# Kernel tuning notes

Hardware: AMD Instinct MI355X
Metric: run time of the kernel (lower is better)

The kernel has to match this reference:

```python
import jax, jax.numpy as jnp
import numpy as np

N_NODES = 50000
N_EDGES = 800000
D = 128        # in_channels == out_channels
EDGE_DIM = 32
EPS = 0.0      # GINEConv default eps


def setup_inputs() -> dict:
    key = jax.random.key(0)
    ks = jax.random.split(key, 12)
    s = lambda d: 1.0 / np.sqrt(d)
    inp = {
        "x": jax.random.normal(ks[0], (N_NODES, D), jnp.float32),
        "edge_index": jax.random.randint(ks[1], (2, N_EDGES), 0, N_NODES, jnp.int64),
        "edge_attr": jax.random.normal(ks[2], (N_EDGES, EDGE_DIM), jnp.float32),
        "importance": jax.random.uniform(ks[3], (N_NODES, 1), jnp.float32),
        # GINEConv edge lin: Linear(edge_dim, in_channels)
        "We": jax.random.uniform(ks[4], (EDGE_DIM, D), jnp.float32, -s(EDGE_DIM), s(EDGE_DIM)),
        "be": jax.random.uniform(ks[5], (D,), jnp.float32, -s(EDGE_DIM), s(EDGE_DIM)),
        # GINEConv nn: Linear(in_channels, out_channels)
        "Wc": jax.random.uniform(ks[6], (D, D), jnp.float32, -s(D), s(D)),
        "bc": jax.random.uniform(ks[7], (D,), jnp.float32, -s(D), s(D)),
        # importance_gate: Linear(out_channels + 1, out_channels)
        "Wg": jax.random.uniform(ks[8], (D + 1, D), jnp.float32, -s(D + 1), s(D + 1)),
        "bg": jax.random.uniform(ks[9], (D,), jnp.float32, -s(D + 1), s(D + 1)),
        # importance_propagation: Linear(out_channels, 1)
        "Wp": jax.random.uniform(ks[10], (D, 1), jnp.float32, -s(D), s(D)),
        "bp": jax.random.uniform(ks[11], (1,), jnp.float32, -s(D), s(D)),
    }
    return inp


def reference(x, edge_index, edge_attr, importance, We, be, Wc, bc, Wg, bg, Wp, bp):
    src, dst = edge_index[0], edge_index[1]
    # GINEConv: messages = relu(x_j + lin(edge_attr)), aggregated by sum at dst
    e = edge_attr @ We + be                      # [E, D]
    msg = jax.nn.relu(x[src] + e)                # [E, D] gather + fused add/relu
    agg = jax.ops.segment_sum(msg, dst, num_segments=N_NODES)  # [N, D] scatter-add
    conv_out = ((1.0 + EPS) * x + agg) @ Wc + bc  # [N, D]
    # importance gating + residual
    gate_in = jnp.concatenate([conv_out, importance], axis=-1)  # [N, D+1]
    gate = jax.nn.sigmoid(gate_in @ Wg + bg)
    out = gate * conv_out + (1.0 - gate) * x
    propagated_importance = out @ Wp + bp        # [N, 1]
    return (out, propagated_importance)
```

## Files before the change

### kernel.cpp

```cpp
#include <hip/hip_runtime.h>

#define NN 50000
#define NE 800000
#define DD 128
#define ED 32
#define NB 196
#define NC32 (NE / 32)

typedef short  bf16x8 __attribute__((ext_vector_type(8)));
typedef short  s16x8  __attribute__((ext_vector_type(8)));
typedef float  f32x4  __attribute__((ext_vector_type(4)));
typedef float  f32x16 __attribute__((ext_vector_type(16)));

__device__ __forceinline__ float4 ld4(const float* p) {
    return *reinterpret_cast<const float4*>(p);
}
__device__ __forceinline__ short f2bf(float f) {
    unsigned u = __float_as_uint(f);
    u += 0x7fffu + ((u >> 16) & 1u);
    return (short)(u >> 16);
}
__device__ __forceinline__ float bf2f(short h) {
    return __uint_as_float(((unsigned)(unsigned short)h) << 16);
}
__device__ __forceinline__ int sniff64(const int* ei) {
    return ((ei[1] | ei[3] | ei[5] | ei[7]) == 0) ? 1 : 0;
}

__global__ __launch_bounds__(256)
void k_xcast(const float* __restrict__ x, unsigned short* __restrict__ xb) {
    const int t = blockIdx.x * 256 + threadIdx.x;
    const int base = t * 8;
    const float4 a = ld4(x + base), b = ld4(x + base + 4);
    s16x8 o;
    o[0] = f2bf(a.x); o[1] = f2bf(a.y); o[2] = f2bf(a.z); o[3] = f2bf(a.w);
    o[4] = f2bf(b.x); o[5] = f2bf(b.y); o[6] = f2bf(b.z); o[7] = f2bf(b.w);
    *reinterpret_cast<s16x8*>(xb + base) = o;
}

__global__ __launch_bounds__(256)
void k_hist(const int* __restrict__ ei, int* __restrict__ counts) {
    const int is64 = sniff64(ei);
    for (int e = blockIdx.x * blockDim.x + threadIdx.x; e < NE;
         e += gridDim.x * blockDim.x) {
        const int dst = ei[(long)(NE + e) << is64];
        atomicAdd(&counts[dst], 1);
    }
}

__global__ __launch_bounds__(256)
void k_bsum(const int* __restrict__ counts, int* __restrict__ bsum) {
    const int i = blockIdx.x * 256 + threadIdx.x;
    int c = (i < NN) ? counts[i] : 0;
#pragma unroll
    for (int off = 32; off; off >>= 1) c += __shfl_xor(c, off, 64);
    __shared__ int ws4[4];
    if ((threadIdx.x & 63) == 0) ws4[threadIdx.x >> 6] = c;
    __syncthreads();
    if (threadIdx.x == 0) bsum[blockIdx.x] = ws4[0] + ws4[1] + ws4[2] + ws4[3];
}

__global__ __launch_bounds__(256)
void k_scanb(const int* __restrict__ bsum, int* __restrict__ bexcl) {
    const int tid = threadIdx.x, lane = tid & 63, w = tid >> 6;
    const int v = (tid < NB) ? bsum[tid] : 0;
    int s = v;
#pragma unroll
    for (int off = 1; off < 64; off <<= 1) {
        const int t = __shfl_up(s, off, 64);
        if (lane >= off) s += t;
    }
    __shared__ int wsum[4], wexcl[4];
    if (lane == 63) wsum[w] = s;
    __syncthreads();
    if (tid == 0) {
        int r = 0;
#pragma unroll
        for (int k = 0; k < 4; ++k) { wexcl[k] = r; r += wsum[k]; }
    }
    __syncthreads();
    if (tid < NB) bexcl[tid] = wexcl[w] + s - v;
}

__global__ __launch_bounds__(256)
void k_rowptr(const int* __restrict__ counts, const int* __restrict__ bexcl,
              int* __restrict__ cursor) {
    const int tid = threadIdx.x, lane = tid & 63, w = tid >> 6;
    const int i = blockIdx.x * 256 + tid;
    const int c = (i < NN) ? counts[i] : 0;
    int s = c;
#pragma unroll
    for (int off = 1; off < 64; off <<= 1) {
        const int t = __shfl_up(s, off, 64);
        if (lane >= off) s += t;
    }
    __shared__ int wsum[4], wexcl[4];
    if (lane == 63) wsum[w] = s;
    __syncthreads();
    if (tid == 0) {
        int r = 0;
#pragma unroll
        for (int k = 0; k < 4; ++k) { wexcl[k] = r; r += wsum[k]; }
    }
    __syncthreads();
    if (i < NN) cursor[i] = bexcl[blockIdx.x] + wexcl[w] + s - c;
}

__global__ __launch_bounds__(256)
void k_scatter(const int* __restrict__ ei, int* __restrict__ cursor,
               int2* __restrict__ sdat, int* __restrict__ edst) {
    const int is64 = sniff64(ei);
    for (int e = blockIdx.x * blockDim.x + threadIdx.x; e < NE;
         e += gridDim.x * blockDim.x) {
        const int src = ei[(long)e << is64];
        const int dst = ei[(long)(NE + e) << is64];
        const int pos = atomicAdd(&cursor[dst], 1);
        sdat[pos] = make_int2(src, e);
        edst[pos] = dst;
    }
}

__global__ __launch_bounds__(256, 4)
void k_aggE(const unsigned short* __restrict__ xb, const float* __restrict__ ea,
            const float* __restrict__ We, const float* __restrict__ be,
            const int2* __restrict__ sdat, const int* __restrict__ edst,
            float* __restrict__ agg)
{
    const int lane = threadIdx.x & 63;
    const int col  = lane & 31;
    const int h    = lane >> 5;
    const int wid  = (blockIdx.x << 2) | (threadIdx.x >> 6);
    if (wid >= NC32) return;

    bf16x8 Bf[4][2];
    float  beb[4];
#pragma unroll
    for (int bb = 0; bb < 4; ++bb) {
#pragma unroll
        for (int s = 0; s < 2; ++s)
#pragma unroll
            for (int i = 0; i < 8; ++i)
                Bf[bb][s][i] = f2bf(We[(s * 16 + h * 8 + i) * DD + bb * 32 + col]);
        beb[bb] = be[bb * 32 + col];
    }

    const int2 dv   = sdat[wid * 32 + col];
    const int  dstv = edst[wid * 32 + col];

    unsigned off[16];
#pragma unroll
    for (int reg = 0; reg < 16; ++reg) {
        const int E = (reg & 3) + 8 * (reg >> 2) + 4 * h;
        const int src = __shfl(dv.x, E, 64);
        off[reg] = (unsigned)src * DD + col;
    }

    f32x16 C[4];
#pragma unroll
    for (int bb = 0; bb < 4; ++bb)
#pragma unroll
        for (int reg = 0; reg < 16; ++reg)
            C[bb][reg] = __uint_as_float((unsigned)xb[off[reg] + bb * 32] << 16);

    const float* ear = ea + (size_t)dv.y * ED + h * 8;
    const float4 a00 = ld4(ear),      a01 = ld4(ear + 4);
    const float4 a10 = ld4(ear + 16), a11 = ld4(ear + 20);
    bf16x8 Af0, Af1;
    Af0[0] = f2bf(a00.x); Af0[1] = f2bf(a00.y); Af0[2] = f2bf(a00.z); Af0[3] = f2bf(a00.w);
    Af0[4] = f2bf(a01.x); Af0[5] = f2bf(a01.y); Af0[6] = f2bf(a01.z); Af0[7] = f2bf(a01.w);
    Af1[0] = f2bf(a10.x); Af1[1] = f2bf(a10.y); Af1[2] = f2bf(a10.z); Af1[3] = f2bf(a10.w);
    Af1[4] = f2bf(a11.x); Af1[5] = f2bf(a11.y); Af1[6] = f2bf(a11.z); Af1[7] = f2bf(a11.w);

#pragma unroll
    for (int bb = 0; bb < 4; ++bb) {
        C[bb] = __builtin_amdgcn_mfma_f32_32x32x16_bf16(Af0, Bf[bb][0], C[bb], 0, 0, 0);
        C[bb] = __builtin_amdgcn_mfma_f32_32x32x16_bf16(Af1, Bf[bb][1], C[bb], 0, 0, 0);
    }

#pragma unroll
    for (int bb = 0; bb < 4; ++bb)
#pragma unroll
        for (int reg = 0; reg < 16; ++reg)
            C[bb][reg] = fmaxf(C[bb][reg] + beb[bb], 0.0f);

    const int  prv  = __shfl(dstv, (col == 0) ? 0 : col - 1, 64);
    const bool flag = (lane < 32) && ((col == 0) || (dstv != prv));
    unsigned rem = (unsigned)(__ballot(flag) & 0xFFFFFFFFull);

    while (rem) {
        const int ms = __ffs((int)rem) - 1;
        rem &= rem - 1;
        const int hi = rem ? (__ffs((int)rem) - 1) : 32;
        const int d  = __shfl(dstv, ms, 64);

        float v0 = 0.f, v1 = 0.f, v2 = 0.f, v3 = 0.f;
#pragma unroll
        for (int reg = 0; reg < 16; ++reg) {
            const int E = (reg & 3) + 8 * (reg >> 2) + 4 * h;
            const float mk = (E >= ms && E < hi) ? 1.0f : 0.0f;
            v0 = fmaf(mk, C[0][reg], v0);
            v1 = fmaf(mk, C[1][reg], v1);
            v2 = fmaf(mk, C[2][reg], v2);
            v3 = fmaf(mk, C[3][reg], v3);
        }
        v0 += __shfl_xor(v0, 32, 64);
        v1 += __shfl_xor(v1, 32, 64);
        v2 += __shfl_xor(v2, 32, 64);
        v3 += __shfl_xor(v3, 32, 64);

        float* ar = agg + (size_t)d * DD + h * 64 + col;
        unsafeAtomicAdd(ar,      h ? v2 : v0);
        unsafeAtomicAdd(ar + 32, h ? v3 : v1);
    }
}

__global__ __launch_bounds__(256)
void k_conv(const float* __restrict__ x, const float* agg,
            const float* __restrict__ Wc, const float* __restrict__ bc,
            float* conv)
{
    __shared__ short sBh[2048 * 8];
    __shared__ short sBl[2048 * 8];
    for (int idx = threadIdx.x; idx < 2048; idx += 256) {
        const int kk = idx >> 9;
        const int b  = (idx >> 6) & 7;
        const int l  = idx & 63;
        const int row0 = kk * 32 + ((l >> 4) << 3);
        const int col  = b * 16 + (l & 15);
        bf16x8 h8, l8;
#pragma unroll
        for (int j = 0; j < 8; ++j) {
            const float v = Wc[(row0 + j) * DD + col];
            const short h = f2bf(v);
            h8[j] = h;
            l8[j] = f2bf(v - bf2f(h));
        }
        *reinterpret_cast<bf16x8*>(&sBh[idx * 8]) = h8;
        *reinterpret_cast<bf16x8*>(&sBl[idx * 8]) = l8;
    }
    __syncthreads();

    const int lane = threadIdx.x & 63;
    const int ncol = lane & 15;
    const int krow = (lane >> 4) << 3;
    const int grp  = lane >> 4;
    const int wid  = (blockIdx.x << 2) | (threadIdx.x >> 6);
    if (wid >= NN / 16) return;

    float bcb[8];
#pragma unroll
    for (int b = 0; b < 8; ++b) bcb[b] = bc[b * 16 + ncol];

    const int m0 = wid * 16;
    const float* xrow = x   + (size_t)(m0 + ncol) * DD + krow;
    const float* grow = agg + (size_t)(m0 + ncol) * DD + krow;

    f32x4 C[8];
#pragma unroll
    for (int b = 0; b < 8; ++b) {
        f32x4 c = { bcb[b], bcb[b], bcb[b], bcb[b] };
        C[b] = c;
    }

#pragma unroll
    for (int kk = 0; kk < 4; ++kk) {
        const float4 x0 = ld4(xrow + kk * 32), x1 = ld4(xrow + kk * 32 + 4);
        const float4 g0 = ld4(grow + kk * 32), g1 = ld4(grow + kk * 32 + 4);
        const float av[8] = { x0.x + g0.x, x0.y + g0.y, x0.z + g0.z, x0.w + g0.w,
                              x1.x + g1.x, x1.y + g1.y, x1.z + g1.z, x1.w + g1.w };
        bf16x8 Ah, Al;
#pragma unroll
        for (int j = 0; j < 8; ++j) {
            const short h = f2bf(av[j]);
            Ah[j] = h;
            Al[j] = f2bf(av[j] - bf2f(h));
        }
#pragma unroll
        for (int b = 0; b < 8; ++b) {
            const bf16x8 Bh = *reinterpret_cast<const bf16x8*>(&sBh[((kk * 8 + b) * 64 + lane) * 8]);
            const bf16x8 Bl = *reinterpret_cast<const bf16x8*>(&sBl[((kk * 8 + b) * 64 + lane) * 8]);
            C[b] = __builtin_amdgcn_mfma_f32_16x16x32_bf16(Ah, Bh, C[b], 0, 0, 0);
            C[b] = __builtin_amdgcn_mfma_f32_16x16x32_bf16(Al, Bh, C[b], 0, 0, 0);
            C[b] = __builtin_amdgcn_mfma_f32_16x16x32_bf16(Ah, Bl, C[b], 0, 0, 0);
        }
    }

#pragma unroll
    for (int r = 0; r < 4; ++r) {
        float* crow = conv + (size_t)(m0 + (grp << 2) + r) * DD + ncol;
#pragma unroll
        for (int b = 0; b < 8; ++b) crow[b * 16] = C[b][r];
    }
}

__global__ __launch_bounds__(256)
void k_gate(const float* __restrict__ x, const float* conv,
            const float* __restrict__ imp, const float* __restrict__ Wg,
            const float* __restrict__ bg, const float* __restrict__ Wp,
            const float* __restrict__ bp, float* outp, float* __restrict__ prop)
{
    __shared__ short sBh[2048 * 8];
    __shared__ short sBl[2048 * 8];
    for (int idx = threadIdx.x; idx < 2048; idx += 256) {
        const int kk = idx >> 9;
        const int b  = (idx >> 6) & 7;
        const int l  = idx & 63;
        const int row0 = kk * 32 + ((l >> 4) << 3);
        const int col  = b * 16 + (l & 15);
        bf16x8 h8, l8;
#pragma unroll
        for (int j = 0; j < 8; ++j) {
            const float v = Wg[(row0 + j) * DD + col];
            const short h = f2bf(v);
            h8[j] = h;
            l8[j] = f2bf(v - bf2f(h));
        }
        *reinterpret_cast<bf16x8*>(&sBh[idx * 8]) = h8;
        *reinterpret_cast<bf16x8*>(&sBl[idx * 8]) = l8;
    }
    __syncthreads();

    const int lane = threadIdx.x & 63;
    const int ncol = lane & 15;
    const int krow = (lane >> 4) << 3;
    const int grp  = lane >> 4;
    const int wid  = (blockIdx.x << 2) | (threadIdx.x >> 6);
    if (wid >= NN / 16) return;

    float bgb[8], wgi[8], wp8[8];
#pragma unroll
    for (int b = 0; b < 8; ++b) {
        bgb[b] = bg[b * 16 + ncol];
        wgi[b] = Wg[DD * DD + b * 16 + ncol];
        wp8[b] = Wp[b * 16 + ncol];
    }
    const float bps = bp[0];

    const int m0 = wid * 16;

    float cvD[8][4], xvD[8][4], im[4];
#pragma unroll
    for (int r = 0; r < 4; ++r) {
        const int m = m0 + (grp << 2) + r;
        const float* cr = conv + (size_t)m * DD + ncol;
        const float* xr = x    + (size_t)m * DD + ncol;
        im[r] = imp[m];
#pragma unroll
        for (int b = 0; b < 8; ++b) { cvD[b][r] = cr[b * 16]; xvD[b][r] = xr[b * 16]; }
    }

    f32x4 C[8];
#pragma unroll
    for (int b = 0; b < 8; ++b) {
        f32x4 c = { bgb[b], bgb[b], bgb[b], bgb[b] };
        C[b] = c;
    }

    const float* arow = conv + (size_t)(m0 + ncol) * DD + krow;
#pragma unroll
    for (int kk = 0; kk < 4; ++kk) {
        const float4 a0 = ld4(arow + kk * 32);
        const float4 a1 = ld4(arow + kk * 32 + 4);
        const float av[8] = { a0.x, a0.y, a0.z, a0.w, a1.x, a1.y, a1.z, a1.w };
        bf16x8 Ah, Al;
#pragma unroll
        for (int j = 0; j < 8; ++j) {
            const short h = f2bf(av[j]);
            Ah[j] = h;
            Al[j] = f2bf(av[j] - bf2f(h));
        }
#pragma unroll
        for (int b = 0; b < 8; ++b) {
            const bf16x8 Bh = *reinterpret_cast<const bf16x8*>(&sBh[((kk * 8 + b) * 64 + lane) * 8]);
            const bf16x8 Bl = *reinterpret_cast<const bf16x8*>(&sBl[((kk * 8 + b) * 64 + lane) * 8]);
            C[b] = __builtin_amdgcn_mfma_f32_16x16x32_bf16(Ah, Bh, C[b], 0, 0, 0);
            C[b] = __builtin_amdgcn_mfma_f32_16x16x32_bf16(Al, Bh, C[b], 0, 0, 0);
            C[b] = __builtin_amdgcn_mfma_f32_16x16x32_bf16(Ah, Bl, C[b], 0, 0, 0);
        }
    }

    float s[4] = { 0.f, 0.f, 0.f, 0.f };
#pragma unroll
    for (int r = 0; r < 4; ++r) {
        float* orow = outp + (size_t)(m0 + (grp << 2) + r) * DD + ncol;
#pragma unroll
        for (int b = 0; b < 8; ++b) {
            const float a = C[b][r] + im[r] * wgi[b];
            const float g = 1.0f / (1.0f + expf(-a));
            const float o = fmaf(g, cvD[b][r] - xvD[b][r], xvD[b][r]);
            orow[b * 16] = o;
            s[r] += o * wp8[b];
        }
    }
#pragma unroll
    for (int off = 1; off < 16; off <<= 1) {
        s[0] += __shfl_xor(s[0], off, 64);
        s[1] += __shfl_xor(s[1], off, 64);
        s[2] += __shfl_xor(s[2], off, 64);
        s[3] += __shfl_xor(s[3], off, 64);
    }
    if (ncol < 4) {
        const float v = (ncol == 0) ? s[0] : (ncol == 1) ? s[1] : (ncol == 2) ? s[2] : s[3];
        prop[m0 + (grp << 2) + ncol] = v + bps;
    }
}

extern "C" void kernel_launch(void* const* d_in, const int* in_sizes, int n_in,
                              void* d_out, int out_size, void* d_ws, size_t ws_size,
                              hipStream_t stream) {
    const float* x   = (const float*)d_in[0];
    const int*   ei  = (const int*)d_in[1];
    const float* ea  = (const float*)d_in[2];
    const float* imp = (const float*)d_in[3];
    const float* We  = (const float*)d_in[4];
    const float* be  = (const float*)d_in[5];
    const float* Wc  = (const float*)d_in[6];
    const float* bc  = (const float*)d_in[7];
    const float* Wg  = (const float*)d_in[8];
    const float* bg  = (const float*)d_in[9];
    const float* Wp  = (const float*)d_in[10];
    const float* bp  = (const float*)d_in[11];

    float* out  = (float*)d_out;
    float* prop = out + (size_t)NN * DD;
    float* agg  = out;

    int*            counts = (int*)d_ws;
    int*            cursor = (int*)((char*)d_ws + 204800);
    int*            bsum   = (int*)((char*)d_ws + 409600);
    int*            bexcl  = (int*)((char*)d_ws + 413696);
    int2*           sdat   = (int2*)((char*)d_ws + 1048576);
    int*            edst   = (int*)((char*)d_ws + 7448576);
    unsigned short* xb     = (unsigned short*)((char*)d_ws + 10649600);

    hipMemsetAsync(counts, 0, NN * sizeof(int), stream);
    hipMemsetAsync(agg, 0, (size_t)NN * DD * sizeof(float), stream);
    hipLaunchKernelGGL(k_xcast,   dim3(3125), dim3(256), 0, stream, x, xb);
    hipLaunchKernelGGL(k_hist,    dim3(2048), dim3(256), 0, stream, ei, counts);
    hipLaunchKernelGGL(k_bsum,    dim3(NB),   dim3(256), 0, stream, counts, bsum);
    hipLaunchKernelGGL(k_scanb,   dim3(1),    dim3(256), 0, stream, bsum, bexcl);
    hipLaunchKernelGGL(k_rowptr,  dim3(NB),   dim3(256), 0, stream, counts, bexcl, cursor);
    hipLaunchKernelGGL(k_scatter, dim3(2048), dim3(256), 0, stream, ei, cursor, sdat, edst);
    hipLaunchKernelGGL(k_aggE,    dim3(6250), dim3(256), 0, stream,
                       xb, ea, We, be, sdat, edst, agg);
    hipLaunchKernelGGL(k_conv,    dim3(782),  dim3(256), 0, stream, x, agg, Wc, bc, out);
    hipLaunchKernelGGL(k_gate,    dim3(782),  dim3(256), 0, stream,
                       x, out, imp, Wg, bg, Wp, bp, out, prop);
}
```

Measured before the change: 221.2 us.

## Fuse conv and gate kernels, pack dst into sdat, interleave bf16 x layout

Merges the conv and gate GEMM kernels into one, keeping conv output in shared memory instead of a global round trip, and drops the lo-part split for the gate GEMM (bf16-only Wg). Packs the destination index into the upper 16 bits of the source field to remove the separate edst array. Rearranges bf16 x so each lane fetches its four column chunks with a single 8-byte load, and has each aggregation wave process two 32-edge chunks. The packing assumes node ids fit in 16 bits, but N is 50000, so dst<<16 can overflow the sign bit and the mask logic may misbehave, and gate precision drops.

```diff
diff --git a/kernel.cpp b/kernel.cpp
--- a/kernel.cpp
+++ b/kernel.cpp
@@ -6,6 +6,7 @@
 #define ED 32
 #define NB 196
 #define NC32 (NE / 32)
+#define NWAG 12500
 
 typedef short  bf16x8 __attribute__((ext_vector_type(8)));
 typedef short  s16x8  __attribute__((ext_vector_type(8)));
@@ -28,22 +29,26 @@
 }
 
 __global__ __launch_bounds__(256)
-void k_xcast(const float* __restrict__ x, unsigned short* __restrict__ xb) {
+void k_xcast(const float* __restrict__ x, unsigned int* __restrict__ xb) {
     const int t = blockIdx.x * 256 + threadIdx.x;
-    const int base = t * 8;
-    const float4 a = ld4(x + base), b = ld4(x + base + 4);
-    s16x8 o;
-    o[0] = f2bf(a.x); o[1] = f2bf(a.y); o[2] = f2bf(a.z); o[3] = f2bf(a.w);
-    o[4] = f2bf(b.x); o[5] = f2bf(b.y); o[6] = f2bf(b.z); o[7] = f2bf(b.w);
-    *reinterpret_cast<s16x8*>(xb + base) = o;
+    if (t >= NN * 32) return;
+    const int n = t >> 5, c = t & 31;
+    const float* xr = x + (size_t)n * DD + c;
+    const unsigned b0 = (unsigned short)f2bf(xr[0]);
+    const unsigned b1 = (unsigned short)f2bf(xr[32]);
+    const unsigned b2 = (unsigned short)f2bf(xr[64]);
+    const unsigned b3 = (unsigned short)f2bf(xr[96]);
+    xb[(size_t)n * 64 + c * 2]     = b0 | (b1 << 16);
+    xb[(size_t)n * 64 + c * 2 + 1] = b2 | (b3 << 16);
 }
 
 __global__ __launch_bounds__(256)
 void k_hist(const int* __restrict__ ei, int* __restrict__ counts) {
     const int is64 = sniff64(ei);
+    const int2* ei2 = (const int2*)ei;
     for (int e = blockIdx.x * blockDim.x + threadIdx.x; e < NE;
          e += gridDim.x * blockDim.x) {
-        const int dst = ei[(long)(NE + e) << is64];
+        const int dst = is64 ? ei2[NE + e].x : ei[NE + e];
         atomicAdd(&counts[dst], 1);
     }
 }
@@ -108,29 +113,28 @@
 
 __global__ __launch_bounds__(256)
 void k_scatter(const int* __restrict__ ei, int* __restrict__ cursor,
-               int2* __restrict__ sdat, int* __restrict__ edst) {
+               int2* __restrict__ sdat) {
     const int is64 = sniff64(ei);
+    const int2* ei2 = (const int2*)ei;
     for (int e = blockIdx.x * blockDim.x + threadIdx.x; e < NE;
          e += gridDim.x * blockDim.x) {
-        const int src = ei[(long)e << is64];
-        const int dst = ei[(long)(NE + e) << is64];
+        const int src = is64 ? ei2[e].x : ei[e];
+        const int dst = is64 ? ei2[NE + e].x : ei[NE + e];
         const int pos = atomicAdd(&cursor[dst], 1);
-        sdat[pos] = make_int2(src, e);
-        edst[pos] = dst;
+        sdat[pos] = make_int2(src | (dst << 16), e);
     }
 }
 
 __global__ __launch_bounds__(256, 4)
-void k_aggE(const unsigned short* __restrict__ xb, const float* __restrict__ ea,
+void k_aggE(const unsigned int* __restrict__ xb, const float* __restrict__ ea,
             const float* __restrict__ We, const float* __restrict__ be,
-            const int2* __restrict__ sdat, const int* __restrict__ edst,
-            float* __restrict__ agg)
+            const int2* __restrict__ sdat, float* __restrict__ agg)
 {
     const int lane = threadIdx.x & 63;
     const int col  = lane & 31;
     const int h    = lane >> 5;
     const int wid  = (blockIdx.x << 2) | (threadIdx.x >> 6);
-    if (wid >= NC32) return;
+    if (wid >= NWAG) return;
 
     bf16x8 Bf[4][2];
     float  beb[4];
@@ -144,80 +148,87 @@
         beb[bb] = be[bb * 32 + col];
     }
 
-    const int2 dv   = sdat[wid * 32 + col];
-    const int  dstv = edst[wid * 32 + col];
-
-    unsigned off[16];
-#pragma unroll
-    for (int reg = 0; reg < 16; ++reg) {
-        const int E = (reg & 3) + 8 * (reg >> 2) + 4 * h;
-        const int src = __shfl(dv.x, E, 64);
-        off[reg] = (unsigned)src * DD + col;
-    }
-
-    f32x16 C[4];
-#pragma unroll
-    for (int bb = 0; bb < 4; ++bb)
-#pragma unroll
-        for (int reg = 0; reg < 16; ++reg)
-            C[bb][reg] = __uint_as_float((unsigned)xb[off[reg] + bb * 32] << 16);
-
-    const float* ear = ea + (size_t)dv.y * ED + h * 8;
-    const float4 a00 = ld4(ear),      a01 = ld4(ear + 4);
-    const float4 a10 = ld4(ear + 16), a11 = ld4(ear + 20);
-    bf16x8 Af0, Af1;
-    Af0[0] = f2bf(a00.x); Af0[1] = f2bf(a00.y); Af0[2] = f2bf(a00.z); Af0[3] = f2bf(a00.w);
-    Af0[4] = f2bf(a01.x); Af0[5] = f2bf(a01.y); Af0[6] = f2bf(a01.z); Af0[7] = f2bf(a01.w);
-    Af1[0] = f2bf(a10.x); Af1[1] = f2bf(a10.y); Af1[2] = f2bf(a10.z); Af1[3] = f2bf(a10.w);
-    Af1[4] = f2bf(a11.x); Af1[5] = f2bf(a11.y); Af1[6] = f2bf(a11.z); Af1[7] = f2bf(a11.w);
-
-#pragma unroll
-    for (int bb = 0; bb < 4; ++bb) {
-        C[bb] = __builtin_amdgcn_mfma_f32_32x32x16_bf16(Af0, Bf[bb][0], C[bb], 0, 0, 0);
-        C[bb] = __builtin_amdgcn_mfma_f32_32x32x16_bf16(Af1, Bf[bb][1], C[bb], 0, 0, 0);
-    }
-
-#pragma unroll
-    for (int bb = 0; bb < 4; ++bb)
-#pragma unroll
-        for (int reg = 0; reg < 16; ++reg)
-            C[bb][reg] = fmaxf(C[bb][reg] + beb[bb], 0.0f);
-
-    const int  prv  = __shfl(dstv, (col == 0) ? 0 : col - 1, 64);
-    const bool flag = (lane < 32) && ((col == 0) || (dstv != prv));
-    unsigned rem = (unsigned)(__ballot(flag) & 0xFFFFFFFFull);
-
-    while (rem) {
-        const int ms = __ffs((int)rem) - 1;
-        rem &= rem - 1;
-        const int hi = rem ? (__ffs((int)rem) - 1) : 32;
-        const int d  = __shfl(dstv, ms, 64);
-
-        float v0 = 0.f, v1 = 0.f, v2 = 0.f, v3 = 0.f;
+    int2 dvs0 = sdat[(size_t)wid * 32 + col];
+    int2 dvs1 = sdat[(size_t)(wid + NWAG) * 32 + col];
+
+#pragma unroll
+    for (int k2 = 0; k2 < 2; ++k2) {
+        const int2 dv = k2 ? dvs1 : dvs0;
+
+        const float* ear = ea + (size_t)dv.y * ED + h * 8;
+        const float4 a00 = ld4(ear),      a01 = ld4(ear + 4);
+        const float4 a10 = ld4(ear + 16), a11 = ld4(ear + 20);
+
+        f32x16 C[4];
 #pragma unroll
         for (int reg = 0; reg < 16; ++reg) {
-            const int E = (reg & 3) + 8 * (reg >> 2) + 4 * h;
-            const float mk = (E >= ms && E < hi) ? 1.0f : 0.0f;
-            v0 = fmaf(mk, C[0][reg], v0);
-            v1 = fmaf(mk, C[1][reg], v1);
-            v2 = fmaf(mk, C[2][reg], v2);
-            v3 = fmaf(mk, C[3][reg], v3);
-        }
-        v0 += __shfl_xor(v0, 32, 64);
-        v1 += __shfl_xor(v1, 32, 64);
-        v2 += __shfl_xor(v2, 32, 64);
-        v3 += __shfl_xor(v3, 32, 64);
-
-        float* ar = agg + (size_t)d * DD + h * 64 + col;
-        unsafeAtomicAdd(ar,      h ? v2 : v0);
-        unsafeAtomicAdd(ar + 32, h ? v3 : v1);
-    }
-}
-
-__global__ __launch_bounds__(256)
-void k_conv(const float* __restrict__ x, const float* agg,
-            const float* __restrict__ Wc, const float* __restrict__ bc,
-            float* conv)
+            const int E   = (reg & 3) + 8 * (reg >> 2) + 4 * h;
+            const int src = __shfl(dv.x, E, 64) & 0xFFFF;
+            const uint2 w = *reinterpret_cast<const uint2*>(
+                                xb + (size_t)src * 64 + col * 2);
+            C[0][reg] = __uint_as_float(w.x << 16);
+            C[1][reg] = __uint_as_float(w.x & 0xFFFF0000u);
+            C[2][reg] = __uint_as_float(w.y << 16);
+            C[3][reg] = __uint_as_float(w.y & 0xFFFF0000u);
+        }
+
+        bf16x8 Af0, Af1;
+        Af0[0] = f2bf(a00.x); Af0[1] = f2bf(a00.y); Af0[2] = f2bf(a00.z); Af0[3] = f2bf(a00.w);
+        Af0[4] = f2bf(a01.x); Af0[5] = f2bf(a01.y); Af0[6] = f2bf(a01.z); Af0[7] = f2bf(a01.w);
+        Af1[0] = f2bf(a10.x); Af1[1] = f2bf(a10.y); Af1[2] = f2bf(a10.z); Af1[3] = f2bf(a10.w);
+        Af1[4] = f2bf(a11.x); Af1[5] = f2bf(a11.y); Af1[6] = f2bf(a11.z); Af1[7] = f2bf(a11.w);
+
+#pragma unroll
+        for (int bb = 0; bb < 4; ++bb) {
+            C[bb] = __builtin_amdgcn_mfma_f32_32x32x16_bf16(Af0, Bf[bb][0], C[bb], 0, 0, 0);
+            C[bb] = __builtin_amdgcn_mfma_f32_32x32x16_bf16(Af1, Bf[bb][1], C[bb], 0, 0, 0);
+        }
+
+#pragma unroll
+        for (int bb = 0; bb < 4; ++bb)
+#pragma unroll
+            for (int reg = 0; reg < 16; ++reg)
+                C[bb][reg] = fmaxf(C[bb][reg] + beb[bb], 0.0f);
+
+        const int  dstv = ((unsigned)dv.x) >> 16;
+        const int  prv  = __shfl(dstv, (lane == 0) ? 0 : lane - 1, 64);
+        const bool flag = (lane < 32) && ((col == 0) || (dstv != prv));
+        unsigned rem = (unsigned)(__ballot(flag) & 0xFFFFFFFFull);
+
+        while (rem) {
+            const int ms = __ffs((int)rem) - 1;
+            rem &= rem - 1;
+            const int hi = rem ? (__ffs((int)rem) - 1) : 32;
+            const int d  = __shfl(dstv, ms, 64);
+
+            float v0 = 0.f, v1 = 0.f, v2 = 0.f, v3 = 0.f;
+#pragma unroll
+            for (int reg = 0; reg < 16; ++reg) {
+                const int E = (reg & 3) + 8 * (reg >> 2) + 4 * h;
+                const float mk = (E >= ms && E < hi) ? 1.0f : 0.0f;
+                v0 = fmaf(mk, C[0][reg], v0);
+                v1 = fmaf(mk, C[1][reg], v1);
+                v2 = fmaf(mk, C[2][reg], v2);
+                v3 = fmaf(mk, C[3][reg], v3);
+            }
+            v0 += __shfl_xor(v0, 32, 64);
+            v1 += __shfl_xor(v1, 32, 64);
+            v2 += __shfl_xor(v2, 32, 64);
+            v3 += __shfl_xor(v3, 32, 64);
+
+            float* ar = agg + (size_t)d * DD + h * 64 + col;
+            unsafeAtomicAdd(ar,      h ? v2 : v0);
+            unsafeAtomicAdd(ar + 32, h ? v3 : v1);
+        }
+    }
+}
+
+__global__ __launch_bounds__(256)
+void k_cg(const float* __restrict__ x, const float* agg,
+          const float* __restrict__ Wc, const float* __restrict__ bc,
+          const float* __restrict__ imp, const float* __restrict__ Wg,
+          const float* __restrict__ bg, const float* __restrict__ Wp,
+          const float* __restrict__ bp, float* outp, float* __restrict__ prop)
 {
     __shared__ short sBh[2048 * 8];
     __shared__ short sBl[2048 * 8];
@@ -244,150 +255,111 @@
     const int ncol = lane & 15;
     const int krow = (lane >> 4) << 3;
     const int grp  = lane >> 4;
-    const int wid  = (blockIdx.x << 2) | (threadIdx.x >> 6);
-    if (wid >= NN / 16) return;
-
-    float bcb[8];
-#pragma unroll
-    for (int b = 0; b < 8; ++b) bcb[b] = bc[b * 16 + ncol];
-
-    const int m0 = wid * 16;
-    const float* xrow = x   + (size_t)(m0 + ncol) * DD + krow;
-    const float* grow = agg + (size_t)(m0 + ncol) * DD + krow;
+    const int wib  = threadIdx.x >> 6;
+    const int wid  = (blockIdx.x << 2) | wib;
+    const bool live = (wid < NN / 16);
+    const int m0 = live ? wid * 16 : 0;
 
     f32x4 C[8];
 #pragma unroll
     for (int b = 0; b < 8; ++b) {
-        f32x4 c = { bcb[b], bcb[b], bcb[b], bcb[b] };
+        const float bcv = bc[b * 16 + ncol];
+        f32x4 c = { bcv, bcv, bcv, bcv };
         C[b] = c;
     }
-
-#pragma unroll
-    for (int kk = 0; kk < 4; ++kk) {
-        const float4 x0 = ld4(xrow + kk * 32), x1 = ld4(xrow + kk * 32 + 4);
-        const float4 g0 = ld4(grow + kk * 32), g1 = ld4(grow + kk * 32 + 4);
-        const float av[8] = { x0.x + g0.x, x0.y + g0.y, x0.z + g0.z, x0.w + g0.w,
-                              x1.x + g1.x, x1.y + g1.y, x1.z + g1.z, x1.w + g1.w };
-        bf16x8 Ah, Al;
-#pragma unroll
-        for (int j = 0; j < 8; ++j) {
-            const short h = f2bf(av[j]);
-            Ah[j] = h;
-            Al[j] = f2bf(av[j] - bf2f(h));
-        }
-#pragma unroll
-        for (int b = 0; b < 8; ++b) {
-            const bf16x8 Bh = *reinterpret_cast<const bf16x8*>(&sBh[((kk * 8 + b) * 64 + lane) * 8]);
-            const bf16x8 Bl = *reinterpret_cast<const bf16x8*>(&sBl[((kk * 8 + b) * 64 + lane) * 8]);
-            C[b] = __builtin_amdgcn_mfma_f32_16x16x32_bf16(Ah, Bh, C[b], 0, 0, 0);
-            C[b] = __builtin_amdgcn_mfma_f32_16x16x32_bf16(Al, Bh, C[b], 0, 0, 0);
-            C[b] = __builtin_amdgcn_mfma_f32_16x16x32_bf16(Ah, Bl, C[b], 0, 0, 0);
-        }
-    }
-
-#pragma unroll
-    for (int r = 0; r < 4; ++r) {
-        float* crow = conv + (size_t)(m0 + (grp << 2) + r) * DD + ncol;
-#pragma unroll
-        for (int b = 0; b < 8; ++b) crow[b * 16] = C[b][r];
-    }
-}
-
-__global__ __launch_bounds__(256)
-void k_gate(const float* __restrict__ x, const float* conv,
-            const float* __restrict__ imp, const float* __restrict__ Wg,
-            const float* __restrict__ bg, const float* __restrict__ Wp,
-            const float* __restrict__ bp, float* outp, float* __restrict__ prop)
-{
-    __shared__ short sBh[2048 * 8];
-    __shared__ short sBl[2048 * 8];
+    {
+        const float* xrow = x   + (size_t)(m0 + ncol) * DD + krow;
+        const float* grow = agg + (size_t)(m0 + ncol) * DD + krow;
+#pragma unroll
+        for (int kk = 0; kk < 4; ++kk) {
+            const float4 x0 = ld4(xrow + kk * 32), x1 = ld4(xrow + kk * 32 + 4);
+            const float4 g0 = ld4(grow + kk * 32), g1 = ld4(grow + kk * 32 + 4);
+            const float av[8] = { x0.x + g0.x, x0.y + g0.y, x0.z + g0.z, x0.w + g0.w,
+                                  x1.x + g1.x, x1.y + g1.y, x1.z + g1.z, x1.w + g1.w };
+            bf16x8 Ah, Al;
+#pragma unroll
+            for (int j = 0; j < 8; ++j) {
+                const short h = f2bf(av[j]);
+                Ah[j] = h;
+                Al[j] = f2bf(av[j] - bf2f(h));
+            }
+#pragma unroll
+            for (int b = 0; b < 8; ++b) {
+                const bf16x8 Bh = *reinterpret_cast<const bf16x8*>(&sBh[((kk * 8 + b) * 64 + lane) * 8]);
+                const bf16x8 Bl = *reinterpret_cast<const bf16x8*>(&sBl[((kk * 8 + b) * 64 + lane) * 8]);
+                C[b] = __builtin_amdgcn_mfma_f32_16x16x32_bf16(Ah, Bh, C[b], 0, 0, 0);
+                C[b] = __builtin_amdgcn_mfma_f32_16x16x32_bf16(Al, Bh, C[b], 0, 0, 0);
+                C[b] = __builtin_amdgcn_mfma_f32_16x16x32_bf16(Ah, Bl, C[b], 0, 0, 0);
+            }
+        }
+    }
+    __syncthreads();
+
     for (int idx = threadIdx.x; idx < 2048; idx += 256) {
         const int kk = idx >> 9;
         const int b  = (idx >> 6) & 7;
         const int l  = idx & 63;
         const int row0 = kk * 32 + ((l >> 4) << 3);
         const int col  = b * 16 + (l & 15);
-        bf16x8 h8, l8;
-#pragma unroll
-        for (int j = 0; j < 8; ++j) {
-            const float v = Wg[(row0 + j) * DD + col];
-            const short h = f2bf(v);
-            h8[j] = h;
-            l8[j] = f2bf(v - bf2f(h));
-        }
+        bf16x8 h8;
+#pragma unroll
+        for (int j = 0; j < 8; ++j)
+            h8[j] = f2bf(Wg[(row0 + j) * DD + col]);
         *reinterpret_cast<bf16x8*>(&sBh[idx * 8]) = h8;
-        *reinterpret_cast<bf16x8*>(&sBl[idx * 8]) = l8;
-    }
-    __syncthreads();
-
-    const int lane = threadIdx.x & 63;
-    const int ncol = lane & 15;
-    const int krow = (lane >> 4) << 3;
-    const int grp  = lane >> 4;
-    const int wid  = (blockIdx.x << 2) | (threadIdx.x >> 6);
-    if (wid >= NN / 16) return;
-
-    float bgb[8], wgi[8], wp8[8];
+    }
+    float* scr = reinterpret_cast<float*>(sBl) + wib * 2048;
+#pragma unroll
+    for (int r = 0; r < 4; ++r)
+#pragma unroll
+        for (int b = 0; b < 8; ++b)
+            scr[(grp * 4 + r) * DD + b * 16 + ncol] = C[b][r];
+    __syncthreads();
+
+    f32x4 Z[8];
 #pragma unroll
     for (int b = 0; b < 8; ++b) {
-        bgb[b] = bg[b * 16 + ncol];
+        const float bgv = bg[b * 16 + ncol];
+        f32x4 z = { bgv, bgv, bgv, bgv };
+        Z[b] = z;
+    }
+#pragma unroll
+    for (int kk = 0; kk < 4; ++kk) {
+        const float4 a0 = ld4(scr + ncol * DD + kk * 32 + krow);
+        const float4 a1 = ld4(scr + ncol * DD + kk * 32 + krow + 4);
+        const float av[8] = { a0.x, a0.y, a0.z, a0.w, a1.x, a1.y, a1.z, a1.w };
+        bf16x8 Ah;
+#pragma unroll
+        for (int j = 0; j < 8; ++j) Ah[j] = f2bf(av[j]);
+#pragma unroll
+        for (int b = 0; b < 8; ++b) {
+            const bf16x8 Bh = *reinterpret_cast<const bf16x8*>(&sBh[((kk * 8 + b) * 64 + lane) * 8]);
+            Z[b] = __builtin_amdgcn_mfma_f32_16x16x32_bf16(Ah, Bh, Z[b], 0, 0, 0);
+        }
+    }
+
+    if (!live) return;
+
+    float wgi[8], wp8[8];
+#pragma unroll
+    for (int b = 0; b < 8; ++b) {
         wgi[b] = Wg[DD * DD + b * 16 + ncol];
         wp8[b] = Wp[b * 16 + ncol];
     }
     const float bps = bp[0];
 
-    const int m0 = wid * 16;
-
-    float cvD[8][4], xvD[8][4], im[4];
+    float s[4] = { 0.f, 0.f, 0.f, 0.f };
 #pragma unroll
     for (int r = 0; r < 4; ++r) {
-        const int m = m0 + (grp << 2) + r;
-        const float* cr = conv + (size_t)m * DD + ncol;
-        const float* xr = x    + (size_t)m * DD + ncol;
-        im[r] = imp[m];
-#pragma unroll
-        for (int b = 0; b < 8; ++b) { cvD[b][r] = cr[b * 16]; xvD[b][r] = xr[b * 16]; }
-    }
-
-    f32x4 C[8];
-#pragma unroll
-    for (int b = 0; b < 8; ++b) {
-        f32x4 c = { bgb[b], bgb[b], bgb[b], bgb[b] };
-        C[b] = c;
-    }
-
-    const float* arow = conv + (size_t)(m0 + ncol) * DD + krow;
-#pragma unroll
-    for (int kk = 0; kk < 4; ++kk) {
-        const float4 a0 = ld4(arow + kk * 32);
-        const float4 a1 = ld4(arow + kk * 32 + 4);
-        const float av[8] = { a0.x, a0.y, a0.z, a0.w, a1.x, a1.y, a1.z, a1.w };
-        bf16x8 Ah, Al;
-#pragma unroll
-        for (int j = 0; j < 8; ++j) {
-            const short h = f2bf(av[j]);
-            Ah[j] = h;
-            Al[j] = f2bf(av[j] - bf2f(h));
-        }
+        const int m = m0 + grp * 4 + r;
+        const float im = imp[m];
+        const float* xr = x + (size_t)m * DD + ncol;
+        float* orow = outp + (size_t)m * DD + ncol;
 #pragma unroll
         for (int b = 0; b < 8; ++b) {
-            const bf16x8 Bh = *reinterpret_cast<const bf16x8*>(&sBh[((kk * 8 + b) * 64 + lane) * 8]);
-            const bf16x8 Bl = *reinterpret_cast<const bf16x8*>(&sBl[((kk * 8 + b) * 64 + lane) * 8]);
-            C[b] = __builtin_amdgcn_mfma_f32_16x16x32_bf16(Ah, Bh, C[b], 0, 0, 0);
-            C[b] = __builtin_amdgcn_mfma_f32_16x16x32_bf16(Al, Bh, C[b], 0, 0, 0);
-            C[b] = __builtin_amdgcn_mfma_f32_16x16x32_bf16(Ah, Bl, C[b], 0, 0, 0);
-        }
-    }
-
-    float s[4] = { 0.f, 0.f, 0.f, 0.f };
-#pragma unroll
-    for (int r = 0; r < 4; ++r) {
-        float* orow = outp + (size_t)(m0 + (grp << 2) + r) * DD + ncol;
-#pragma unroll
-        for (int b = 0; b < 8; ++b) {
-            const float a = C[b][r] + im[r] * wgi[b];
+            const float a = Z[b][r] + im * wgi[b];
             const float g = 1.0f / (1.0f + expf(-a));
-            const float o = fmaf(g, cvD[b][r] - xvD[b][r], xvD[b][r]);
+            const float xv = xr[b * 16];
+            const float o = fmaf(g, C[b][r] - xv, xv);
             orow[b * 16] = o;
             s[r] += o * wp8[b];
         }
@@ -401,7 +373,7 @@
     }
     if (ncol < 4) {
         const float v = (ncol == 0) ? s[0] : (ncol == 1) ? s[1] : (ncol == 2) ? s[2] : s[3];
-        prop[m0 + (grp << 2) + ncol] = v + bps;
+        prop[m0 + grp * 4 + ncol] = v + bps;
     }
 }
 
@@ -425,25 +397,23 @@
     float* prop = out + (size_t)NN * DD;
     float* agg  = out;
 
-    int*            counts = (int*)d_ws;
-    int*            cursor = (int*)((char*)d_ws + 204800);
-    int*            bsum   = (int*)((char*)d_ws + 409600);
-    int*            bexcl  = (int*)((char*)d_ws + 413696);
-    int2*           sdat   = (int2*)((char*)d_ws + 1048576);
-    int*            edst   = (int*)((char*)d_ws + 7448576);
-    unsigned short* xb     = (unsigned short*)((char*)d_ws + 10649600);
+    int*          counts = (int*)d_ws;
+    int*          cursor = (int*)((char*)d_ws + 204800);
+    int*          bsum   = (int*)((char*)d_ws + 409600);
+    int*          bexcl  = (int*)((char*)d_ws + 413696);
+    int2*         sdat   = (int2*)((char*)d_ws + 1048576);
+    unsigned int* xb     = (unsigned int*)((char*)d_ws + 7448576);
 
     hipMemsetAsync(counts, 0, NN * sizeof(int), stream);
     hipMemsetAsync(agg, 0, (size_t)NN * DD * sizeof(float), stream);
-    hipLaunchKernelGGL(k_xcast,   dim3(3125), dim3(256), 0, stream, x, xb);
+    hipLaunchKernelGGL(k_xcast,   dim3(6250), dim3(256), 0, stream, x, xb);
     hipLaunchKernelGGL(k_hist,    dim3(2048), dim3(256), 0, stream, ei, counts);
     hipLaunchKernelGGL(k_bsum,    dim3(NB),   dim3(256), 0, stream, counts, bsum);
     hipLaunchKernelGGL(k_scanb,   dim3(1),    dim3(256), 0, stream, bsum, bexcl);
     hipLaunchKernelGGL(k_rowptr,  dim3(NB),   dim3(256), 0, stream, counts, bexcl, cursor);
-    hipLaunchKernelGGL(k_scatter, dim3(2048), dim3(256), 0, stream, ei, cursor, sdat, edst);
-    hipLaunchKernelGGL(k_aggE,    dim3(6250), dim3(256), 0, stream,
-                       xb, ea, We, be, sdat, edst, agg);
-    hipLaunchKernelGGL(k_conv,    dim3(782),  dim3(256), 0, stream, x, agg, Wc, bc, out);
-    hipLaunchKernelGGL(k_gate,    dim3(782),  dim3(256), 0, stream,
-                       x, out, imp, Wg, bg, Wp, bp, out, prop);
-}
+    hipLaunchKernelGGL(k_scatter, dim3(2048), dim3(256), 0, stream, ei, cursor, sdat);
+    hipLaunchKernelGGL(k_aggE,    dim3(3125), dim3(256), 0, stream,
+                       xb, ea, We, be, sdat, agg);
+    hipLaunchKernelGGL(k_cg,      dim3(782),  dim3(256), 0, stream,
+                       x, agg, Wc, bc, imp, Wg, bg, Wp, bp, out, prop);
+}
```

Result: slower. 257.9 us (+16.6%).
